# Kernel optimization log

Hardware: AMD Instinct MI355X
Metric: run time of the kernel (lower is better)

## Reference

```python
import jax, jax.numpy as jnp
import numpy as np

N_ENSEMBLE = 50
STATE_DIM = 32
ACTION_DIM = 8
HIDDEN = 256
BATCH = 8192
OUT_DIM = STATE_DIM + 1  # next_state + reward


def setup_inputs() -> dict:
    key = jax.random.key(0)
    ks = jax.random.split(key, 8)
    s = 0.05  # small init scale to keep activations sane
    return {
        "state": jax.random.normal(ks[0], (BATCH, STATE_DIM), dtype=jnp.float32),
        "action": jax.random.normal(ks[1], (BATCH, ACTION_DIM), dtype=jnp.float32),
        "W1": jax.random.normal(ks[2], (N_ENSEMBLE, STATE_DIM + ACTION_DIM, HIDDEN), dtype=jnp.float32) * s,
        "b1": jnp.zeros((N_ENSEMBLE, HIDDEN), dtype=jnp.float32),
        "W2": jax.random.normal(ks[3], (N_ENSEMBLE, HIDDEN, HIDDEN), dtype=jnp.float32) * s,
        "b2": jnp.zeros((N_ENSEMBLE, HIDDEN), dtype=jnp.float32),
        "W3": jax.random.normal(ks[4], (N_ENSEMBLE, HIDDEN, HIDDEN), dtype=jnp.float32) * s,
        "b3": jnp.zeros((N_ENSEMBLE, HIDDEN), dtype=jnp.float32),
        "W4": jax.random.normal(ks[5], (N_ENSEMBLE, HIDDEN, OUT_DIM), dtype=jnp.float32) * s,
        "b4": jnp.zeros((N_ENSEMBLE, OUT_DIM), dtype=jnp.float32),
    }


def reference(state, action, W1, b1, W2, b2, W3, b3, W4, b4):
    # state_action: [B, S+A] shared across all ensemble members
    sa = jnp.concatenate((state, action), axis=1)
    # Batched-over-ensemble GEMMs replace the python loop over 50 MLPs.
    # h: [B, E, H]
    h = jax.nn.relu(jnp.einsum("bi,eih->beh", sa, W1) + b1)
    h = jax.nn.relu(jnp.einsum("beh,ehk->bek", h, W2) + b2)
    h = jax.nn.relu(jnp.einsum("beh,ehk->bek", h, W3) + b3)
    preds = jnp.einsum("beh,eho->beo", h, W4) + b4  # [B, E, S+1]
    return preds[..., :-1], preds[..., -1]
```

## Files before the change

kernel.cpp:

```cpp
#include <hip/hip_runtime.h>


typedef __attribute__((ext_vector_type(8))) short short8;
typedef __attribute__((ext_vector_type(4))) float floatx4;

#define NE 50
#define NB 8192
#define OUT_NS_ELEMS (NB * NE * 32)

__device__ __forceinline__ unsigned short f2bf_rne(float x) {
  unsigned u = __float_as_uint(x);
  u += 0x7fffu + ((u >> 16) & 1u);
  return (unsigned short)(u >> 16);
}
__device__ __forceinline__ float bf2f(unsigned short b) {
  return __uint_as_float(((unsigned)b) << 16);
}
__device__ __forceinline__ floatx4 mfma16(short8 a, short8 b, floatx4 c) {
  return __builtin_amdgcn_mfma_f32_16x16x32_bf16(a, b, c, 0, 0, 0);
}
__device__ __forceinline__ unsigned pack_bf2(float lo, float hi) {
  unsigned u0 = __float_as_uint(lo) + 0x8000u;
  unsigned u1 = __float_as_uint(hi) + 0x8000u;
  return __builtin_amdgcn_perm(u1, u0, 0x07060302u);
}

__global__ void k_init_flag(int* flag) { *flag = 1; }

__global__ void k_detect(const unsigned* __restrict__ w2raw, int* __restrict__ flag) {
  int tid = blockIdx.x * 256 + threadIdx.x;
  bool bad = false;
  for (int i = tid; i < 1638400; i += 256 * 256) {
    unsigned word = w2raw[i];
    unsigned short lo = (unsigned short)(word & 0xFFFFu);
    float f = bf2f(lo);
    if (!(fabsf(f) < 16.0f)) bad = true;
    if (lo == 0) bad = true;
  }
  if (bad) *flag = 0;
}

__device__ __forceinline__ unsigned short load_bf(const void* p, long i, bool isbf) {
  if (isbf) return ((const unsigned short*)p)[i];
  return f2bf_rne(((const float*)p)[i]);
}
__device__ __forceinline__ float load_f(const void* p, long i, bool isbf) {
  if (isbf) return bf2f(((const unsigned short*)p)[i]);
  return ((const float*)p)[i];
}

__device__ void pack_w_panel(const void* __restrict__ src, unsigned short* __restrict__ dst,
                             bool isbf, int e, int kt, int K, int N, int NT, int perE,
                             unsigned short* lds) {
  const int t = threadIdx.x;
  const int Npad = NT * 16;
  const int NP = Npad + 10;
  for (int idx = t; idx < 32 * Npad; idx += 256) {
    int r = idx / Npad, c = idx - r * Npad;
    int k = kt * 32 + r;
    unsigned short v = 0;
    if (k < K && c < N) v = load_bf(src, (long)(e * K + k) * N + c, isbf);
    lds[r * NP + c] = v;
  }
  __syncthreads();
  for (int u = t; u < NT * 64; u += 256) {
    int nt = u >> 6, kb = (u >> 4) & 3, ni = u & 15;
    int n = nt * 16 + ni;
    unsigned v[4];
#pragma unroll
    for (int p = 0; p < 4; ++p) {
      unsigned lo = lds[(kb * 8 + 2 * p) * NP + n];
      unsigned hi = lds[(kb * 8 + 2 * p + 1) * NP + n];
      v[p] = lo | (hi << 16);
    }
    long off = (long)e * perE + ((long)((kt * NT + nt) * 64 + kb * 16 + ni)) * 8;
    *(uint4*)(dst + off) = make_uint4(v[0], v[1], v[2], v[3]);
  }
}

__global__ void k_pack(const void* __restrict__ state, const void* __restrict__ action,
                       const void* __restrict__ W1, const void* __restrict__ W2,
                       const void* __restrict__ W3, const void* __restrict__ W4,
                       const void* __restrict__ b1, const void* __restrict__ b2,
                       const void* __restrict__ b3, const void* __restrict__ b4,
                       const int* __restrict__ flag,
                       unsigned short* __restrict__ saP, unsigned short* __restrict__ w1P,
                       unsigned short* __restrict__ w2P, unsigned short* __restrict__ w3P,
                       unsigned short* __restrict__ w4P, float* __restrict__ biasP) {
  __shared__ unsigned short lds[32 * 266];
  const bool isbf = (*flag != 0);
  const int b = blockIdx.x;
  if (b < 400) {
    pack_w_panel(W2, w2P, isbf, b >> 3, b & 7, 256, 256, 16, 65536, lds);
  } else if (b < 800) {
    int bb = b - 400;
    pack_w_panel(W3, w3P, isbf, bb >> 3, bb & 7, 256, 256, 16, 65536, lds);
  } else if (b < 900) {
    int bb = b - 800;
    pack_w_panel(W1, w1P, isbf, bb >> 1, bb & 1, 40, 256, 16, 16384, lds);
  } else if (b < 1300) {
    int bb = b - 900;
    pack_w_panel(W4, w4P, isbf, bb >> 3, bb & 7, 256, 33, 3, 12288, lds);
  } else if (b < 1556) {
    int u = (b - 1300) * 256 + threadIdx.x;
    int mi = u & 15, kb = (u >> 4) & 7, mt = u >> 7;
    int row = mt * 16 + mi;
    unsigned v[4] = {0u, 0u, 0u, 0u};
    if (kb < 4) {
#pragma unroll
      for (int p = 0; p < 4; ++p) {
        unsigned lo = load_bf(state, (long)row * 32 + kb * 8 + 2 * p, isbf);
        unsigned hi = load_bf(state, (long)row * 32 + kb * 8 + 2 * p + 1, isbf);
        v[p] = lo | (hi << 16);
      }
    } else if (kb == 4) {
#pragma unroll
      for (int p = 0; p < 4; ++p) {
        unsigned lo = load_bf(action, (long)row * 8 + 2 * p, isbf);
        unsigned hi = load_bf(action, (long)row * 8 + 2 * p + 1, isbf);
        v[p] = lo | (hi << 16);
      }
    }
    *(uint4*)(saP + (long)u * 8) = make_uint4(v[0], v[1], v[2], v[3]);
  } else {
    int gid = (b - 1556) * 256 + threadIdx.x;
    if (gid < NE * 816) {
      int e = gid / 816, r = gid - e * 816;
      float v = 0.0f;
      if (r < 256)      v = load_f(b1, e * 256 + r,         isbf);
      else if (r < 512) v = load_f(b2, e * 256 + (r - 256), isbf);
      else if (r < 768) v = load_f(b3, e * 256 + (r - 512), isbf);
      else { int q = r - 768; if (q < 33) v = load_f(b4, e * 33 + q, isbf); }
      biasP[gid] = v;
    }
  }
}


__device__ __forceinline__ void store_hT(const floatx4 (&acc)[4][4], unsigned short* hT,
                                         int w, int li, int g) {
#pragma unroll
  for (int ot = 0; ot < 4; ++ot) {
    int k0 = w * 64 + ot * 16 + g * 4;
    int base = ((k0 >> 5) * 4) * 512 + ((k0 >> 3) & 3) * 128 + li * 8 + (k0 & 7);
#pragma unroll
    for (int bt = 0; bt < 4; ++bt) {
      float v0 = fmaxf(acc[ot][bt][0], 0.0f);
      float v1 = fmaxf(acc[ot][bt][1], 0.0f);
      float v2 = fmaxf(acc[ot][bt][2], 0.0f);
      float v3 = fmaxf(acc[ot][bt][3], 0.0f);
      unsigned d0 = pack_bf2(v0, v1);
      unsigned d1 = pack_bf2(v2, v3);
      *(unsigned long long*)(hT + base + bt * 512) =
          (unsigned long long)d0 | ((unsigned long long)d1 << 32);
    }
  }
}

__device__ __forceinline__ void bias_init(floatx4 (&acc)[4][4], const float* br,
                                          int w, int g) {
#pragma unroll
  for (int ot = 0; ot < 4; ++ot) {
    const float4 b4 = *(const float4*)(br + w * 64 + ot * 16 + g * 4);
    floatx4 iv = {b4.x, b4.y, b4.z, b4.w};
#pragma unroll
    for (int bt = 0; bt < 4; ++bt) acc[ot][bt] = iv;
  }
}

__device__ __forceinline__ void hidden_layer(const unsigned short* __restrict__ wb,
                                             const float* __restrict__ br,
                                             unsigned short* hT, int w, int l, int li, int g) {
  floatx4 acc[4][4];
  bias_init(acc, br, w, g);
  for (int kt = 0; kt < 8; ++kt) {
    short8 a[4], b[4];
#pragma unroll
    for (int ot = 0; ot < 4; ++ot)
      a[ot] = *(const short8*)(wb + (long)((kt * 16 + w * 4 + ot) * 64 + l) * 8);
#pragma unroll
    for (int bt = 0; bt < 4; ++bt)
      b[bt] = *(const short8*)(hT + ((kt * 4 + bt) * 64 + l) * 8);
#pragma unroll
    for (int ot = 0; ot < 4; ++ot)
#pragma unroll
      for (int bt = 0; bt < 4; ++bt)
        acc[ot][bt] = mfma16(a[ot], b[bt], acc[ot][bt]);
  }
  __syncthreads();
  store_hT(acc, hT, w, li, g);
  __syncthreads();
}

__global__ __launch_bounds__(256, 4) void k_mlp(
    const unsigned short* __restrict__ sa,
    const unsigned short* __restrict__ w1,
    const unsigned short* __restrict__ w2,
    const unsigned short* __restrict__ w3,
    const unsigned short* __restrict__ w4,
    const float* __restrict__ bias,
    const int* __restrict__ flag,
    void* __restrict__ outp) {
  __shared__ __attribute__((aligned(16))) unsigned short hT[16384];
  const int tid = threadIdx.x;
  const int w = tid >> 6, l = tid & 63, li = l & 15, g = l >> 4;
  const int bb = blockIdx.x;
  const int e  = blockIdx.y;
  const float* brow = bias + e * 816;
  const bool isbf = (*flag != 0);

  {
    floatx4 acc[4][4];
    bias_init(acc, brow, w, g);
#pragma unroll
    for (int kt = 0; kt < 2; ++kt) {
      short8 a[4], b[4];
#pragma unroll
      for (int ot = 0; ot < 4; ++ot)
        a[ot] = *(const short8*)(w1 + (long)e * 16384 + (long)((kt * 16 + w * 4 + ot) * 64 + l) * 8);
#pragma unroll
      for (int bt = 0; bt < 4; ++bt)
        b[bt] = *(const short8*)(sa + (long)((bb * 4 + bt) * 128 + kt * 64 + l) * 8);
#pragma unroll
      for (int ot = 0; ot < 4; ++ot)
#pragma unroll
        for (int bt = 0; bt < 4; ++bt)
          acc[ot][bt] = mfma16(a[ot], b[bt], acc[ot][bt]);
    }
    store_hT(acc, hT, w, li, g);
    __syncthreads();
  }

  hidden_layer(w2 + (long)e * 65536, brow + 256, hT, w, l, li, g);
  hidden_layer(w3 + (long)e * 65536, brow + 512, hT, w, l, li, g);

  const float* brow4 = brow + 768;
  floatx4 acc4[3];
#pragma unroll
  for (int ot = 0; ot < 3; ++ot) {
    const float4 b4 = *(const float4*)(brow4 + ot * 16 + g * 4);
    acc4[ot] = (floatx4){b4.x, b4.y, b4.z, b4.w};
  }
  for (int kt = 0; kt < 8; ++kt) {
    short8 bfrag = *(const short8*)(hT + ((kt * 4 + w) * 64 + l) * 8);
#pragma unroll
    for (int ot = 0; ot < 3; ++ot) {
      short8 a = *(const short8*)(w4 + (long)e * 12288 + (long)((kt * 3 + ot) * 64 + l) * 8);
      acc4[ot] = mfma16(a, bfrag, acc4[ot]);
    }
  }

  const int batch = bb * 64 + w * 16 + li;
  const long nsbase = (long)(batch * NE + e) * 32;
  if (isbf) {
    unsigned short* o16 = (unsigned short*)outp;
#pragma unroll
    for (int ot = 0; ot < 2; ++ot) {
      unsigned d0 = pack_bf2(acc4[ot][0], acc4[ot][1]);
      unsigned d1 = pack_bf2(acc4[ot][2], acc4[ot][3]);
      *(unsigned long long*)(o16 + nsbase + ot * 16 + g * 4) =
          (unsigned long long)d0 | ((unsigned long long)d1 << 32);
    }
    if (g == 0) {
      unsigned u = __float_as_uint(acc4[2][0]) + 0x8000u;
      o16[OUT_NS_ELEMS + batch * NE + e] = (unsigned short)(u >> 16);
    }
  } else {
    float* o32 = (float*)outp;
#pragma unroll
    for (int ot = 0; ot < 2; ++ot)
      *(float4*)(o32 + nsbase + ot * 16 + g * 4) =
          make_float4(acc4[ot][0], acc4[ot][1], acc4[ot][2], acc4[ot][3]);
    if (g == 0) o32[OUT_NS_ELEMS + batch * NE + e] = acc4[2][0];
  }
}

extern "C" void kernel_launch(void* const* d_in, const int* in_sizes, int n_in,
                              void* d_out, int out_size, void* d_ws, size_t ws_size,
                              hipStream_t stream) {
  const void* state  = d_in[0];
  const void* action = d_in[1];
  const void* W1 = d_in[2];
  const void* b1 = d_in[3];
  const void* W2 = d_in[4];
  const void* b2 = d_in[5];
  const void* W3 = d_in[6];
  const void* b3 = d_in[7];
  const void* W4 = d_in[8];
  const void* b4 = d_in[9];
  (void)in_sizes; (void)n_in; (void)out_size; (void)ws_size;

  char* ws = (char*)d_ws;
  int* flag              = (int*)(ws + 0);
  unsigned short* saP    = (unsigned short*)(ws + 256);
  unsigned short* w1P    = (unsigned short*)(ws + 1048832);
  unsigned short* w2P    = (unsigned short*)(ws + 2687232);
  unsigned short* w3P    = (unsigned short*)(ws + 9240832);
  unsigned short* w4P    = (unsigned short*)(ws + 15794432);
  float* biasP           = (float*)(ws + 17023232);

  k_init_flag<<<1, 1, 0, stream>>>(flag);
  k_detect<<<256, 256, 0, stream>>>((const unsigned*)W2, flag);
  k_pack<<<1716, 256, 0, stream>>>(state, action, W1, W2, W3, W4, b1, b2, b3, b4,
                                   flag, saP, w1P, w2P, w3P, w4P, biasP);
  k_mlp<<<dim3(128, 50), 256, 0, stream>>>(saP, w1P, w2P, w3P, w4P, biasP, flag, d_out);
}
```

Before: 268.1 us.

## Double batch tile per block to 128 rows with 512 threads, prefetch weights, shrink dtype probe

The MLP kernel now uses 512-thread blocks that each cover 128 batch rows. The 8 waves are split into 4 feature groups times 2 batch groups, so each weight fragment loaded from global memory serves twice as many batch rows, and the activation buffer in shared memory doubles to 64KB. The hidden-layer loop now prefetches the next k-step's weight fragments into registers before issuing the MFMAs. Separately, the dtype-detection kernel is cut to a single block that samples 2048 strided words, and the flag-init launch is dropped. The costs are higher register and LDS pressure per block and fewer blocks in flight, and the sampled probe could misdetect the input dtype.

Result: faster. 261.4 us (-2.5%).

```diff
diff --git a/kernel.cpp b/kernel.cpp
--- a/kernel.cpp
+++ b/kernel.cpp
@@ -25,19 +25,21 @@
   return __builtin_amdgcn_perm(u1, u0, 0x07060302u);
 }
 
-__global__ void k_init_flag(int* flag) { *flag = 1; }
-
 __global__ void k_detect(const unsigned* __restrict__ w2raw, int* __restrict__ flag) {
-  int tid = blockIdx.x * 256 + threadIdx.x;
+  __shared__ int s_bad;
+  if (threadIdx.x == 0) s_bad = 0;
+  __syncthreads();
   bool bad = false;
-  for (int i = tid; i < 1638400; i += 256 * 256) {
-    unsigned word = w2raw[i];
+  for (int i = threadIdx.x; i < 2048; i += 256) {
+    unsigned word = w2raw[i * 797];
     unsigned short lo = (unsigned short)(word & 0xFFFFu);
     float f = bf2f(lo);
     if (!(fabsf(f) < 16.0f)) bad = true;
     if (lo == 0) bad = true;
   }
-  if (bad) *flag = 0;
+  if (bad) s_bad = 1;
+  __syncthreads();
+  if (threadIdx.x == 0) *flag = s_bad ? 0 : 1;
 }
 
 __device__ __forceinline__ unsigned short load_bf(const void* p, long i, bool isbf) {
@@ -138,11 +140,11 @@
 
 
 __device__ __forceinline__ void store_hT(const floatx4 (&acc)[4][4], unsigned short* hT,
-                                         int w, int li, int g) {
+                                         int wf, int wb, int li, int g) {
 #pragma unroll
   for (int ot = 0; ot < 4; ++ot) {
-    int k0 = w * 64 + ot * 16 + g * 4;
-    int base = ((k0 >> 5) * 4) * 512 + ((k0 >> 3) & 3) * 128 + li * 8 + (k0 & 7);
+    int k0 = wf * 64 + ot * 16 + g * 4;
+    int base = ((k0 >> 5) * 8) * 512 + ((k0 >> 3) & 3) * 128 + li * 8 + (k0 & 7);
 #pragma unroll
     for (int bt = 0; bt < 4; ++bt) {
       float v0 = fmaxf(acc[ot][bt][0], 0.0f);
@@ -151,48 +153,59 @@
       float v3 = fmaxf(acc[ot][bt][3], 0.0f);
       unsigned d0 = pack_bf2(v0, v1);
       unsigned d1 = pack_bf2(v2, v3);
-      *(unsigned long long*)(hT + base + bt * 512) =
+      *(unsigned long long*)(hT + base + (wb * 4 + bt) * 512) =
           (unsigned long long)d0 | ((unsigned long long)d1 << 32);
     }
   }
 }
 
 __device__ __forceinline__ void bias_init(floatx4 (&acc)[4][4], const float* br,
-                                          int w, int g) {
+                                          int wf, int g) {
 #pragma unroll
   for (int ot = 0; ot < 4; ++ot) {
-    const float4 b4 = *(const float4*)(br + w * 64 + ot * 16 + g * 4);
+    const float4 b4 = *(const float4*)(br + wf * 64 + ot * 16 + g * 4);
     floatx4 iv = {b4.x, b4.y, b4.z, b4.w};
 #pragma unroll
     for (int bt = 0; bt < 4; ++bt) acc[ot][bt] = iv;
   }
 }
 
-__device__ __forceinline__ void hidden_layer(const unsigned short* __restrict__ wb,
+__device__ __forceinline__ void hidden_layer(const unsigned short* __restrict__ wb_ptr,
                                              const float* __restrict__ br,
-                                             unsigned short* hT, int w, int l, int li, int g) {
+                                             unsigned short* hT,
+                                             int wf, int wb, int l, int li, int g) {
   floatx4 acc[4][4];
-  bias_init(acc, br, w, g);
+  bias_init(acc, br, wf, g);
+  short8 a[4], an[4], b[4];
+#pragma unroll
+  for (int ot = 0; ot < 4; ++ot)
+    a[ot] = *(const short8*)(wb_ptr + (long)((0 * 16 + wf * 4 + ot) * 64 + l) * 8);
+#pragma unroll
   for (int kt = 0; kt < 8; ++kt) {
-    short8 a[4], b[4];
-#pragma unroll
-    for (int ot = 0; ot < 4; ++ot)
-      a[ot] = *(const short8*)(wb + (long)((kt * 16 + w * 4 + ot) * 64 + l) * 8);
+    if (kt < 7) {
+#pragma unroll
+      for (int ot = 0; ot < 4; ++ot)
+        an[ot] = *(const short8*)(wb_ptr + (long)(((kt + 1) * 16 + wf * 4 + ot) * 64 + l) * 8);
+    }
 #pragma unroll
     for (int bt = 0; bt < 4; ++bt)
-      b[bt] = *(const short8*)(hT + ((kt * 4 + bt) * 64 + l) * 8);
+      b[bt] = *(const short8*)(hT + ((kt * 8 + wb * 4 + bt) * 64 + l) * 8);
 #pragma unroll
     for (int ot = 0; ot < 4; ++ot)
 #pragma unroll
       for (int bt = 0; bt < 4; ++bt)
         acc[ot][bt] = mfma16(a[ot], b[bt], acc[ot][bt]);
-  }
-  __syncthreads();
-  store_hT(acc, hT, w, li, g);
-  __syncthreads();
-}
-
-__global__ __launch_bounds__(256, 4) void k_mlp(
+    if (kt < 7) {
+#pragma unroll
+      for (int ot = 0; ot < 4; ++ot) a[ot] = an[ot];
+    }
+  }
+  __syncthreads();
+  store_hT(acc, hT, wf, wb, li, g);
+  __syncthreads();
+}
+
+__global__ __launch_bounds__(512, 4) void k_mlp(
     const unsigned short* __restrict__ sa,
     const unsigned short* __restrict__ w1,
     const unsigned short* __restrict__ w2,
@@ -201,9 +214,10 @@
     const float* __restrict__ bias,
     const int* __restrict__ flag,
     void* __restrict__ outp) {
-  __shared__ __attribute__((aligned(16))) unsigned short hT[16384];
+  __shared__ __attribute__((aligned(16))) unsigned short hT[32768];
   const int tid = threadIdx.x;
   const int w = tid >> 6, l = tid & 63, li = l & 15, g = l >> 4;
+  const int wf = w & 3, wbk = w >> 2;
   const int bb = blockIdx.x;
   const int e  = blockIdx.y;
   const float* brow = bias + e * 816;
@@ -211,28 +225,29 @@
 
   {
     floatx4 acc[4][4];
-    bias_init(acc, brow, w, g);
+    bias_init(acc, brow, wf, g);
 #pragma unroll
     for (int kt = 0; kt < 2; ++kt) {
       short8 a[4], b[4];
 #pragma unroll
       for (int ot = 0; ot < 4; ++ot)
-        a[ot] = *(const short8*)(w1 + (long)e * 16384 + (long)((kt * 16 + w * 4 + ot) * 64 + l) * 8);
+        a[ot] = *(const short8*)(w1 + (long)e * 16384 +
+                                 (long)((kt * 16 + wf * 4 + ot) * 64 + l) * 8);
 #pragma unroll
       for (int bt = 0; bt < 4; ++bt)
-        b[bt] = *(const short8*)(sa + (long)((bb * 4 + bt) * 128 + kt * 64 + l) * 8);
+        b[bt] = *(const short8*)(sa + (long)((bb * 8 + wbk * 4 + bt) * 128 + kt * 64 + l) * 8);
 #pragma unroll
       for (int ot = 0; ot < 4; ++ot)
 #pragma unroll
         for (int bt = 0; bt < 4; ++bt)
           acc[ot][bt] = mfma16(a[ot], b[bt], acc[ot][bt]);
     }
-    store_hT(acc, hT, w, li, g);
+    store_hT(acc, hT, wf, wbk, li, g);
     __syncthreads();
   }
 
-  hidden_layer(w2 + (long)e * 65536, brow + 256, hT, w, l, li, g);
-  hidden_layer(w3 + (long)e * 65536, brow + 512, hT, w, l, li, g);
+  hidden_layer(w2 + (long)e * 65536, brow + 256, hT, wf, wbk, l, li, g);
+  hidden_layer(w3 + (long)e * 65536, brow + 512, hT, wf, wbk, l, li, g);
 
   const float* brow4 = brow + 768;
   floatx4 acc4[3];
@@ -241,8 +256,9 @@
     const float4 b4 = *(const float4*)(brow4 + ot * 16 + g * 4);
     acc4[ot] = (floatx4){b4.x, b4.y, b4.z, b4.w};
   }
+#pragma unroll
   for (int kt = 0; kt < 8; ++kt) {
-    short8 bfrag = *(const short8*)(hT + ((kt * 4 + w) * 64 + l) * 8);
+    short8 bfrag = *(const short8*)(hT + ((kt * 8 + w) * 64 + l) * 8);
 #pragma unroll
     for (int ot = 0; ot < 3; ++ot) {
       short8 a = *(const short8*)(w4 + (long)e * 12288 + (long)((kt * 3 + ot) * 64 + l) * 8);
@@ -250,7 +266,7 @@
     }
   }
 
-  const int batch = bb * 64 + w * 16 + li;
+  const int batch = bb * 128 + w * 16 + li;
   const long nsbase = (long)(batch * NE + e) * 32;
   if (isbf) {
     unsigned short* o16 = (unsigned short*)outp;
@@ -299,9 +315,8 @@
   unsigned short* w4P    = (unsigned short*)(ws + 15794432);
   float* biasP           = (float*)(ws + 17023232);
 
-  k_init_flag<<<1, 1, 0, stream>>>(flag);
-  k_detect<<<256, 256, 0, stream>>>((const unsigned*)W2, flag);
+  k_detect<<<1, 256, 0, stream>>>((const unsigned*)W2, flag);
   k_pack<<<1716, 256, 0, stream>>>(state, action, W1, W2, W3, W4, b1, b2, b3, b4,
                                    flag, saP, w1P, w2P, w3P, w4P, biasP);
-  k_mlp<<<dim3(128, 50), 256, 0, stream>>>(saP, w1P, w2P, w3P, w4P, biasP, flag, d_out);
-}
+  k_mlp<<<dim3(64, 50), 512, 0, stream>>>(saP, w1P, w2P, w3P, w4P, biasP, flag, d_out);
+}
```
